# Optimization experiments

Hardware: AMD Instinct MI355X
Metric: run time of the kernel (lower is better)

## Reference

```python
import jax, jax.numpy as jnp
import numpy as np

B, C, N = 2, 256, 4096
H, HD = 8, 32  # num_heads, head_dim; H*HD == C
SCALE = HD ** (-0.5)


def setup_inputs() -> dict:
    key = jax.random.key(0)
    ks = jax.random.split(key, 5)
    return {
        "x": jax.random.normal(ks[0], (B, C, N), dtype=jnp.float32),
        "qkv_w": jax.random.normal(ks[1], (3 * C, C), dtype=jnp.float32) * (C ** -0.5),
        "qkv_b": jax.random.normal(ks[2], (3 * C,), dtype=jnp.float32) * 0.02,
        "out_w": jax.random.normal(ks[3], (C, C), dtype=jnp.float32) * (C ** -0.5),
        "out_b": jax.random.normal(ks[4], (C,), dtype=jnp.float32) * 0.02,
    }


def reference(x, qkv_w, qkv_b, out_w, out_b):
    b, c, n = x.shape
    # 1x1 conv == channel GEMM: [b, 3c, n]
    qkv = jnp.einsum("oc,bcn->bon", qkv_w, x) + qkv_b[None, :, None]
    qkv = qkv.reshape(b, 3, H, c // H, n)
    qkv = jnp.transpose(qkv, (1, 0, 2, 4, 3))  # (3, b, h, n, hd)
    q, k, v = qkv[0], qkv[1], qkv[2]
    attn = jnp.einsum("bhqd,bhkd->bhqk", q, k) * SCALE  # full NxN scores
    attn = jax.nn.softmax(attn, axis=-1)
    out = jnp.einsum("bhqk,bhkd->bhqd", attn, v)
    out = jnp.transpose(out, (0, 1, 3, 2)).reshape(b, c, n)
    out = jnp.einsum("oc,bcn->bon", out_w, out) + out_b[None, :, None]
    return out
```

## Files before the change

kernel.cpp:

```cpp
#include <hip/hip_runtime.h>
#include <math.h>

#define NSEQ 4096
#define QSCL (0.17677669529663687f * 1.4426950408889634f)

typedef __attribute__((ext_vector_type(2))) _Float16 half2v;
typedef __attribute__((ext_vector_type(8))) _Float16 half8;
typedef __attribute__((ext_vector_type(4))) float f32x4;
typedef __attribute__((ext_vector_type(16))) float f32x16;
typedef __attribute__((ext_vector_type(2))) float f32x2;
typedef __attribute__((ext_vector_type(2))) unsigned int u32x2;
typedef __attribute__((ext_vector_type(4))) unsigned int u32x4;

#if __has_builtin(__builtin_amdgcn_exp2f)
#define EXP2(x) __builtin_amdgcn_exp2f(x)
#else
#define EXP2(x) exp2f(x)
#endif

__device__ __forceinline__ half2v pk2(float a, float b) {
  return __builtin_bit_cast(half2v, __builtin_amdgcn_cvt_pkrtz(a, b));
}
__device__ __forceinline__ unsigned pk2u(float a, float b) {
  return __builtin_bit_cast(unsigned, __builtin_amdgcn_cvt_pkrtz(a, b));
}

__device__ __forceinline__ void swap32(unsigned a, unsigned b, unsigned& r0,
                                       unsigned& r1, int lane) {
#if __has_builtin(__builtin_amdgcn_permlane32_swap)
  typedef __attribute__((ext_vector_type(2))) unsigned uint2v;
  uint2v s = __builtin_amdgcn_permlane32_swap(a, b, false, false);
  r0 = s[0];
  r1 = s[1];
#else
  unsigned ax = __shfl_xor((int)a, 32), bx = __shfl_xor((int)b, 32);
  const bool lo = lane < 32;
  r0 = lo ? a : bx;
  r1 = lo ? ax : b;
#endif
}

__global__ __launch_bounds__(256) void prep_all(
    const float* __restrict__ x, const float* __restrict__ qkv_w,
    const float* __restrict__ out_w, _Float16* __restrict__ Xh,
    _Float16* __restrict__ Wqh, _Float16* __restrict__ Wql,
    _Float16* __restrict__ Woh, _Float16* __restrict__ Wol) {
  __shared__ float T[64][68];
  if (blockIdx.z == 2) {
    const int wid = blockIdx.y * 64 + blockIdx.x;
    const int idx = (wid * 256 + threadIdx.x) * 4;
    const int NQ = 768 * 256;
    float4 v;
    _Float16 *dh, *dl;
    int off;
    if (idx < NQ) {
      off = idx;
      v = *(const float4*)(qkv_w + off);
      dh = Wqh;
      dl = Wql;
    } else {
      off = idx - NQ;
      v = *(const float4*)(out_w + off);
      dh = Woh;
      dl = Wol;
    }
    half2v h0 = pk2(v.x, v.y), h1 = pk2(v.z, v.w);
    half2v l0 = pk2(v.x - (float)h0[0], v.y - (float)h0[1]);
    half2v l1 = pk2(v.z - (float)h1[0], v.w - (float)h1[1]);
    u32x2 H, L;
    H[0] = __builtin_bit_cast(unsigned, h0);
    H[1] = __builtin_bit_cast(unsigned, h1);
    L[0] = __builtin_bit_cast(unsigned, l0);
    L[1] = __builtin_bit_cast(unsigned, l1);
    *(u32x2*)(dh + off) = H;
    *(u32x2*)(dl + off) = L;
    return;
  }
  const int b = blockIdx.z, c0 = blockIdx.y * 64, n0 = blockIdx.x * 64;
  const int t = threadIdx.x;
  {
    const int cc = t >> 4, nn = (t & 15) * 4;
    #pragma unroll
    for (int i = 0; i < 4; ++i) {
      float4 v = *(const float4*)(x + ((size_t)(b * 256 + c0 + cc + i * 16)) * NSEQ + n0 + nn);
      *(float4*)&T[cc + i * 16][nn] = v;
    }
  }
  __syncthreads();
  const int nn = t >> 2, cq = t & 3;
  float v[16];
  #pragma unroll
  for (int jj = 0; jj < 16; ++jj) v[jj] = T[cq * 16 + jj][nn];
  half8 hi0, hi1;
  #pragma unroll
  for (int i = 0; i < 4; ++i) {
    half2v h = pk2(v[2 * i], v[2 * i + 1]);
    hi0[2 * i] = h[0]; hi0[2 * i + 1] = h[1];
    half2v h2 = pk2(v[8 + 2 * i], v[8 + 2 * i + 1]);
    hi1[2 * i] = h2[0]; hi1[2 * i + 1] = h2[1];
  }
  const size_t base = ((size_t)b * NSEQ + n0 + nn) * 256 + c0 + cq * 16;
  *(half8*)(Xh + base) = hi0;
  *(half8*)(Xh + base + 8) = hi1;
}

__global__ __launch_bounds__(256) void gemm_qkv(
    const _Float16* __restrict__ Wh, const _Float16* __restrict__ Wl,
    const _Float16* __restrict__ Xh, const float* __restrict__ bias,
    _Float16* __restrict__ Qp, _Float16* __restrict__ Kp,
    _Float16* __restrict__ Vp) {
  const int b = blockIdx.z, n0 = blockIdx.x * 64, m0 = blockIdx.y * 128;
  const int tid = threadIdx.x, w = tid >> 6, lane = tid & 63;
  const int lq = lane & 15, g = lane >> 4;
  const int mw = m0 + w * 32;
  f32x4 acc[2][4] = {};
  const size_t a0 = (size_t)(mw + lq) * 256 + 8 * g;
  const size_t a1 = (size_t)(mw + 16 + lq) * 256 + 8 * g;
  const size_t xrow = ((size_t)b * NSEQ + n0 + lq) * 256 + 8 * g;
  #pragma unroll
  for (int k0 = 0; k0 < 256; k0 += 32) {
    half8 ah0 = *(const half8*)(Wh + a0 + k0);
    half8 ah1 = *(const half8*)(Wh + a1 + k0);
    half8 al0 = *(const half8*)(Wl + a0 + k0);
    half8 al1 = *(const half8*)(Wl + a1 + k0);
    #pragma unroll
    for (int ns = 0; ns < 4; ++ns) {
      half8 bh_ = *(const half8*)(Xh + xrow + (size_t)ns * 16 * 256 + k0);
      acc[0][ns] = __builtin_amdgcn_mfma_f32_16x16x32_f16(ah0, bh_, acc[0][ns], 0, 0, 0);
      acc[0][ns] = __builtin_amdgcn_mfma_f32_16x16x32_f16(al0, bh_, acc[0][ns], 0, 0, 0);
      acc[1][ns] = __builtin_amdgcn_mfma_f32_16x16x32_f16(ah1, bh_, acc[1][ns], 0, 0, 0);
      acc[1][ns] = __builtin_amdgcn_mfma_f32_16x16x32_f16(al1, bh_, acc[1][ns], 0, 0, 0);
    }
  }
  const int seg = mw >> 8;
  const int hh = (mw >> 5) & 7;
  const int bhi = b * 8 + hh;
  #pragma unroll
  for (int ms = 0; ms < 2; ++ms) {
    const int dbase = ms * 16 + 4 * g;
    float4 bi = *(const float4*)(bias + mw + dbase);
    #pragma unroll
    for (int ns = 0; ns < 4; ++ns) {
      const int n = n0 + ns * 16 + lq;
      float v0 = acc[ms][ns][0] + bi.x;
      float v1 = acc[ms][ns][1] + bi.y;
      float v2 = acc[ms][ns][2] + bi.z;
      float v3 = acc[ms][ns][3] + bi.w;
      if (seg == 0) {
        v0 *= QSCL; v1 *= QSCL; v2 *= QSCL; v3 *= QSCL;
        u32x2 H;
        H[0] = pk2u(v0, v1);
        H[1] = pk2u(v2, v3);
        *(u32x2*)(Qp + ((size_t)bhi * NSEQ + n) * 32 + dbase) = H;
      } else if (seg == 1) {
        u32x2 H;
        H[0] = pk2u(v0, v1);
        H[1] = pk2u(v2, v3);
        *(u32x2*)(Kp + ((size_t)bhi * NSEQ + n) * 32 + dbase) = H;
      } else {
        Vp[((size_t)bhi * 32 + dbase + 0) * NSEQ + n] = (_Float16)v0;
        Vp[((size_t)bhi * 32 + dbase + 1) * NSEQ + n] = (_Float16)v1;
        Vp[((size_t)bhi * 32 + dbase + 2) * NSEQ + n] = (_Float16)v2;
        Vp[((size_t)bhi * 32 + dbase + 3) * NSEQ + n] = (_Float16)v3;
      }
    }
  }
}

__global__ __launch_bounds__(256, 2) void attn_part(
    const _Float16* __restrict__ Qp, const _Float16* __restrict__ Kp,
    const _Float16* __restrict__ Vp, _Float16* __restrict__ pp,
    float* __restrict__ lsum) {
  const int b = blockIdx.z, h = blockIdx.y, bh = b * 8 + h;
  const int qt = blockIdx.x & 15, ks_ = blockIdx.x >> 4;
  const int tid = threadIdx.x, w = tid >> 6, lane = tid & 63;
  const int l31 = lane & 31, hw = lane >> 5;
  const int hi8 = hw * 8;
  const int n0 = qt * 256 + w * 64;

  half8 qf[2][2];
  #pragma unroll
  for (int s = 0; s < 2; ++s)
    #pragma unroll
    for (int dh = 0; dh < 2; ++dh)
      qf[s][dh] = *(const half8*)(Qp + ((size_t)bh * NSEQ + n0 + s * 32 + l31) * 32 +
                                  dh * 16 + hi8);

  f32x16 acc[2] = {};
  float lp[2][4] = {};
  const _Float16* Kb = Kp + ((size_t)bh * NSEQ + ks_ * 2048) * 32;
  const _Float16* Vb = Vp + (size_t)bh * 32 * NSEQ + ks_ * 2048;

  half8 kA[4], kB[4];

  auto kload = [&](half8* dst, int t) {
    const int key0 = t * 64;
    #pragma unroll
    for (int kt = 0; kt < 2; ++kt)
      #pragma unroll
      for (int dh = 0; dh < 2; ++dh)
        dst[kt * 2 + dh] = *(const half8*)(Kb + (size_t)(key0 + kt * 32 + l31) * 32 +
                                           dh * 16 + hi8);
  };

  auto compute = [&](const half8* kf, int t) {
    const int key0 = t * 64;
    half8 vf[4];
    #pragma unroll
    for (int c = 0; c < 4; ++c)
      vf[c] = *(const half8*)(Vb + (size_t)l31 * NSEQ + key0 + c * 16 + hi8);
    __builtin_amdgcn_s_setprio(1);
    #pragma unroll
    for (int s = 0; s < 2; ++s) {
      #pragma unroll
      for (int kt = 0; kt < 2; ++kt) {
        f32x16 sc = {0.f, 0.f, 0.f, 0.f, 0.f, 0.f, 0.f, 0.f,
                     0.f, 0.f, 0.f, 0.f, 0.f, 0.f, 0.f, 0.f};
        sc = __builtin_amdgcn_mfma_f32_32x32x16_f16(kf[kt * 2 + 0], qf[s][0], sc, 0, 0, 0);
        sc = __builtin_amdgcn_mfma_f32_32x32x16_f16(kf[kt * 2 + 1], qf[s][1], sc, 0, 0, 0);
        float p[16];
        #pragma unroll
        for (int i = 0; i < 16; ++i) {
          p[i] = EXP2(sc[i]);
          lp[s][i & 3] += p[i];
        }
        #pragma unroll
        for (int cc = 0; cc < 2; ++cc) {
          unsigned A01 = pk2u(p[cc * 8 + 0], p[cc * 8 + 1]);
          unsigned A23 = pk2u(p[cc * 8 + 2], p[cc * 8 + 3]);
          unsigned A45 = pk2u(p[cc * 8 + 4], p[cc * 8 + 5]);
          unsigned A67 = pk2u(p[cc * 8 + 6], p[cc * 8 + 7]);
          unsigned r0, r1, r2, r3;
          swap32(A01, A45, r0, r1, lane);
          swap32(A23, A67, r2, r3, lane);
          u32x4 W;
          W[0] = r0;
          W[1] = r2;
          W[2] = r1;
          W[3] = r3;
          half8 pb = __builtin_bit_cast(half8, W);
          acc[s] = __builtin_amdgcn_mfma_f32_32x32x16_f16(vf[kt * 2 + cc], pb, acc[s], 0, 0, 0);
        }
      }
    }
    __builtin_amdgcn_s_setprio(0);
  };

  kload(kA, 0);
  #pragma unroll 1
  for (int t = 0; t < 32; t += 2) {
    kload(kB, t + 1);
    compute(kA, t);
    kload(kA, t + 2 < 32 ? t + 2 : 31);
    compute(kB, t + 1);
  }

  #pragma unroll
  for (int s = 0; s < 2; ++s) {
    float l = (lp[s][0] + lp[s][1]) + (lp[s][2] + lp[s][3]);
    l += __shfl_xor(l, 32);
    const float inv = 1.f / l;
    const int q = n0 + s * 32 + l31;
    const size_t pbase = ((size_t)(bh * 2 + ks_) * NSEQ + q) * 32;
    #pragma unroll
    for (int rg = 0; rg < 4; ++rg) {
      const int d0 = rg * 8 + 4 * hw;
      float v0 = acc[s][rg * 4 + 0] * inv, v1 = acc[s][rg * 4 + 1] * inv;
      float v2 = acc[s][rg * 4 + 2] * inv, v3 = acc[s][rg * 4 + 3] * inv;
      u32x2 H;
      H[0] = pk2u(v0, v1);
      H[1] = pk2u(v2, v3);
      *(u32x2*)(pp + pbase + d0) = H;
    }
    if (lane < 32) lsum[((size_t)bh * NSEQ + q) * 2 + ks_] = l;
  }
}

__global__ __launch_bounds__(256) void gemm_proj(
    const _Float16* __restrict__ Wh, const _Float16* __restrict__ Wl,
    const _Float16* __restrict__ pp, const float* __restrict__ lsum,
    const float* __restrict__ bias, float* __restrict__ out) {
  const int b = blockIdx.z, n0 = blockIdx.x * 64, m0 = blockIdx.y * 64;
  const int tid = threadIdx.x, w = tid >> 6, lane = tid & 63;
  const int lq = lane & 15, g = lane >> 4;
  const int mw = m0 + w * 16;
  f32x4 acc[4] = {};
  const size_t a0 = (size_t)(mw + lq) * 256 + 8 * g;
  #pragma unroll
  for (int k0 = 0; k0 < 256; k0 += 32) {
    half8 ah = *(const half8*)(Wh + a0 + k0);
    half8 al = *(const half8*)(Wl + a0 + k0);
    const int c = k0 + 8 * g;
    const int hch = c >> 5, d0 = c & 31;
    const int bh = b * 8 + hch;
    #pragma unroll
    for (int ns = 0; ns < 4; ++ns) {
      const int n = n0 + ns * 16 + lq;
      const size_t pb = ((size_t)(bh * 2) * NSEQ + n) * 32 + d0;
      half8 pa = *(const half8*)(pp + pb);
      half8 pbp = *(const half8*)(pp + pb + (size_t)NSEQ * 32);
      f32x2 lv = *(const f32x2*)(lsum + ((size_t)bh * NSEQ + n) * 2);
      const float iv = 1.f / (lv[0] + lv[1]);
      const float w0 = lv[0] * iv, w1 = lv[1] * iv;
      half8 bh_;
      #pragma unroll
      for (int i = 0; i < 4; ++i) {
        float e0 = w0 * (float)pa[2 * i] + w1 * (float)pbp[2 * i];
        float e1 = w0 * (float)pa[2 * i + 1] + w1 * (float)pbp[2 * i + 1];
        half2v hp = pk2(e0, e1);
        bh_[2 * i] = hp[0];
        bh_[2 * i + 1] = hp[1];
      }
      acc[ns] = __builtin_amdgcn_mfma_f32_16x16x32_f16(ah, bh_, acc[ns], 0, 0, 0);
      acc[ns] = __builtin_amdgcn_mfma_f32_16x16x32_f16(al, bh_, acc[ns], 0, 0, 0);
    }
  }
  float4 bi = *(const float4*)(bias + mw + 4 * g);
  #pragma unroll
  for (int ns = 0; ns < 4; ++ns) {
    const int n = n0 + ns * 16 + lq;
    out[((size_t)b * 256 + mw + 4 * g + 0) * NSEQ + n] = acc[ns][0] + bi.x;
    out[((size_t)b * 256 + mw + 4 * g + 1) * NSEQ + n] = acc[ns][1] + bi.y;
    out[((size_t)b * 256 + mw + 4 * g + 2) * NSEQ + n] = acc[ns][2] + bi.z;
    out[((size_t)b * 256 + mw + 4 * g + 3) * NSEQ + n] = acc[ns][3] + bi.w;
  }
}

extern "C" void kernel_launch(void* const* d_in, const int* in_sizes, int n_in,
                              void* d_out, int out_size, void* d_ws, size_t ws_size,
                              hipStream_t stream) {
  const float* x = (const float*)d_in[0];
  const float* qkv_w = (const float*)d_in[1];
  const float* qkv_b = (const float*)d_in[2];
  const float* out_w = (const float*)d_in[3];
  const float* out_b = (const float*)d_in[4];
  float* out = (float*)d_out;

  char* ws = (char*)d_ws;
  _Float16* Vp = (_Float16*)(ws);
  _Float16* Qp = (_Float16*)(ws + (4u << 20));
  _Float16* Kp = (_Float16*)(ws + (8u << 20));
  _Float16* Xh = (_Float16*)(ws + (12u << 20));
  _Float16* pp = (_Float16*)(ws + (16u << 20));
  _Float16* Wqh = (_Float16*)(ws + (28u << 20));
  _Float16* Wql = (_Float16*)(ws + (28u << 20) + (384u << 10));
  _Float16* Woh = (_Float16*)(ws + (28u << 20) + (768u << 10));
  _Float16* Wol = (_Float16*)(ws + (28u << 20) + (896u << 10));
  float* lsum = (float*)(ws + (29u << 20));

  prep_all<<<dim3(NSEQ / 64, 4, 3), 256, 0, stream>>>(x, qkv_w, out_w, Xh,
                                                      Wqh, Wql, Woh, Wol);
  gemm_qkv<<<dim3(NSEQ / 64, 6, 2), 256, 0, stream>>>(Wqh, Wql, Xh, qkv_b,
                                                      Qp, Kp, Vp);
  attn_part<<<dim3(32, 8, 2), 256, 0, stream>>>(Qp, Kp, Vp, pp, lsum);
  gemm_proj<<<dim3(NSEQ / 64, 4, 2), 256, 0, stream>>>(Woh, Wol, pp, lsum,
                                                       out_b, out);
}
```

Before: 101.6 us.

## Fuse input and weight fp16 conversion into the GEMM kernels, drop prep kernel

Removes the separate prep kernel. gemm_qkv now loads fp32 x tiles, converts and transposes them through shared memory, and splits fp32 weights into hi/lo halves in registers on the fly. gemm_proj also converts its fp32 weights inline. This saves one launch and the round trip of the converted tensors through global memory. In exchange, every block redoes the weight conversion and adds shared-memory staging with per-chunk barriers, and the scalar 2-byte shared-memory stores may cause bank conflicts.

```diff
diff --git a/kernel.cpp b/kernel.cpp
--- a/kernel.cpp
+++ b/kernel.cpp
@@ -23,6 +23,20 @@
 }
 __device__ __forceinline__ unsigned pk2u(float a, float b) {
   return __builtin_bit_cast(unsigned, __builtin_amdgcn_cvt_pkrtz(a, b));
+}
+
+__device__ __forceinline__ void cvt_hilo(float4 a, float4 b, half8& hi,
+                                         half8& lo) {
+  half2v h0 = pk2(a.x, a.y), h1 = pk2(a.z, a.w);
+  half2v h2 = pk2(b.x, b.y), h3 = pk2(b.z, b.w);
+  hi[0] = h0[0]; hi[1] = h0[1]; hi[2] = h1[0]; hi[3] = h1[1];
+  hi[4] = h2[0]; hi[5] = h2[1]; hi[6] = h3[0]; hi[7] = h3[1];
+  half2v e0 = pk2(a.x - (float)h0[0], a.y - (float)h0[1]);
+  half2v e1 = pk2(a.z - (float)h1[0], a.w - (float)h1[1]);
+  half2v e2 = pk2(b.x - (float)h2[0], b.y - (float)h2[1]);
+  half2v e3 = pk2(b.z - (float)h3[0], b.w - (float)h3[1]);
+  lo[0] = e0[0]; lo[1] = e0[1]; lo[2] = e1[0]; lo[3] = e1[1];
+  lo[4] = e2[0]; lo[5] = e2[1]; lo[6] = e3[0]; lo[7] = e3[1];
 }
 
 __device__ __forceinline__ void swap32(unsigned a, unsigned b, unsigned& r0,
@@ -40,96 +54,52 @@
 #endif
 }
 
-__global__ __launch_bounds__(256) void prep_all(
-    const float* __restrict__ x, const float* __restrict__ qkv_w,
-    const float* __restrict__ out_w, _Float16* __restrict__ Xh,
-    _Float16* __restrict__ Wqh, _Float16* __restrict__ Wql,
-    _Float16* __restrict__ Woh, _Float16* __restrict__ Wol) {
-  __shared__ float T[64][68];
-  if (blockIdx.z == 2) {
-    const int wid = blockIdx.y * 64 + blockIdx.x;
-    const int idx = (wid * 256 + threadIdx.x) * 4;
-    const int NQ = 768 * 256;
-    float4 v;
-    _Float16 *dh, *dl;
-    int off;
-    if (idx < NQ) {
-      off = idx;
-      v = *(const float4*)(qkv_w + off);
-      dh = Wqh;
-      dl = Wql;
-    } else {
-      off = idx - NQ;
-      v = *(const float4*)(out_w + off);
-      dh = Woh;
-      dl = Wol;
-    }
-    half2v h0 = pk2(v.x, v.y), h1 = pk2(v.z, v.w);
-    half2v l0 = pk2(v.x - (float)h0[0], v.y - (float)h0[1]);
-    half2v l1 = pk2(v.z - (float)h1[0], v.w - (float)h1[1]);
-    u32x2 H, L;
-    H[0] = __builtin_bit_cast(unsigned, h0);
-    H[1] = __builtin_bit_cast(unsigned, h1);
-    L[0] = __builtin_bit_cast(unsigned, l0);
-    L[1] = __builtin_bit_cast(unsigned, l1);
-    *(u32x2*)(dh + off) = H;
-    *(u32x2*)(dl + off) = L;
-    return;
-  }
-  const int b = blockIdx.z, c0 = blockIdx.y * 64, n0 = blockIdx.x * 64;
-  const int t = threadIdx.x;
-  {
-    const int cc = t >> 4, nn = (t & 15) * 4;
-    #pragma unroll
-    for (int i = 0; i < 4; ++i) {
-      float4 v = *(const float4*)(x + ((size_t)(b * 256 + c0 + cc + i * 16)) * NSEQ + n0 + nn);
-      *(float4*)&T[cc + i * 16][nn] = v;
-    }
-  }
-  __syncthreads();
-  const int nn = t >> 2, cq = t & 3;
-  float v[16];
-  #pragma unroll
-  for (int jj = 0; jj < 16; ++jj) v[jj] = T[cq * 16 + jj][nn];
-  half8 hi0, hi1;
-  #pragma unroll
-  for (int i = 0; i < 4; ++i) {
-    half2v h = pk2(v[2 * i], v[2 * i + 1]);
-    hi0[2 * i] = h[0]; hi0[2 * i + 1] = h[1];
-    half2v h2 = pk2(v[8 + 2 * i], v[8 + 2 * i + 1]);
-    hi1[2 * i] = h2[0]; hi1[2 * i + 1] = h2[1];
-  }
-  const size_t base = ((size_t)b * NSEQ + n0 + nn) * 256 + c0 + cq * 16;
-  *(half8*)(Xh + base) = hi0;
-  *(half8*)(Xh + base + 8) = hi1;
-}
-
 __global__ __launch_bounds__(256) void gemm_qkv(
-    const _Float16* __restrict__ Wh, const _Float16* __restrict__ Wl,
-    const _Float16* __restrict__ Xh, const float* __restrict__ bias,
-    _Float16* __restrict__ Qp, _Float16* __restrict__ Kp,
-    _Float16* __restrict__ Vp) {
+    const float* __restrict__ Wf, const float* __restrict__ x,
+    const float* __restrict__ bias, _Float16* __restrict__ Qp,
+    _Float16* __restrict__ Kp, _Float16* __restrict__ Vp) {
+  __shared__ _Float16 XT[64][72];
   const int b = blockIdx.z, n0 = blockIdx.x * 64, m0 = blockIdx.y * 128;
   const int tid = threadIdx.x, w = tid >> 6, lane = tid & 63;
   const int lq = lane & 15, g = lane >> 4;
   const int mw = m0 + w * 32;
+  const int cc = tid >> 4, nn = (tid & 15) * 4;
   f32x4 acc[2][4] = {};
-  const size_t a0 = (size_t)(mw + lq) * 256 + 8 * g;
-  const size_t a1 = (size_t)(mw + 16 + lq) * 256 + 8 * g;
-  const size_t xrow = ((size_t)b * NSEQ + n0 + lq) * 256 + 8 * g;
-  #pragma unroll
-  for (int k0 = 0; k0 < 256; k0 += 32) {
-    half8 ah0 = *(const half8*)(Wh + a0 + k0);
-    half8 ah1 = *(const half8*)(Wh + a1 + k0);
-    half8 al0 = *(const half8*)(Wl + a0 + k0);
-    half8 al1 = *(const half8*)(Wl + a1 + k0);
-    #pragma unroll
-    for (int ns = 0; ns < 4; ++ns) {
-      half8 bh_ = *(const half8*)(Xh + xrow + (size_t)ns * 16 * 256 + k0);
-      acc[0][ns] = __builtin_amdgcn_mfma_f32_16x16x32_f16(ah0, bh_, acc[0][ns], 0, 0, 0);
-      acc[0][ns] = __builtin_amdgcn_mfma_f32_16x16x32_f16(al0, bh_, acc[0][ns], 0, 0, 0);
-      acc[1][ns] = __builtin_amdgcn_mfma_f32_16x16x32_f16(ah1, bh_, acc[1][ns], 0, 0, 0);
-      acc[1][ns] = __builtin_amdgcn_mfma_f32_16x16x32_f16(al1, bh_, acc[1][ns], 0, 0, 0);
+  const size_t wr0 = (size_t)(mw + lq) * 256 + 8 * g;
+  const size_t wr1 = (size_t)(mw + 16 + lq) * 256 + 8 * g;
+
+  for (int kc = 0; kc < 4; ++kc) {
+    if (kc) __syncthreads();
+    #pragma unroll
+    for (int i = 0; i < 4; ++i) {
+      const int c = cc + 16 * i;
+      float4 v = *(const float4*)(
+          x + ((size_t)(b * 256 + kc * 64 + c)) * NSEQ + n0 + nn);
+      XT[nn + 0][c] = (_Float16)v.x;
+      XT[nn + 1][c] = (_Float16)v.y;
+      XT[nn + 2][c] = (_Float16)v.z;
+      XT[nn + 3][c] = (_Float16)v.w;
+    }
+    __syncthreads();
+    #pragma unroll
+    for (int kh = 0; kh < 2; ++kh) {
+      const int k0 = kc * 64 + kh * 32;
+      float4 wa0 = *(const float4*)(Wf + wr0 + k0);
+      float4 wa1 = *(const float4*)(Wf + wr0 + k0 + 4);
+      float4 wb0 = *(const float4*)(Wf + wr1 + k0);
+      float4 wb1 = *(const float4*)(Wf + wr1 + k0 + 4);
+      half8 ah0, al0, ah1, al1;
+      cvt_hilo(wa0, wa1, ah0, al0);
+      cvt_hilo(wb0, wb1, ah1, al1);
+      const int dk = kh * 32 + 8 * g;
+      #pragma unroll
+      for (int ns = 0; ns < 4; ++ns) {
+        half8 bh_ = *(const half8*)&XT[ns * 16 + lq][dk];
+        acc[0][ns] = __builtin_amdgcn_mfma_f32_16x16x32_f16(ah0, bh_, acc[0][ns], 0, 0, 0);
+        acc[0][ns] = __builtin_amdgcn_mfma_f32_16x16x32_f16(al0, bh_, acc[0][ns], 0, 0, 0);
+        acc[1][ns] = __builtin_amdgcn_mfma_f32_16x16x32_f16(ah1, bh_, acc[1][ns], 0, 0, 0);
+        acc[1][ns] = __builtin_amdgcn_mfma_f32_16x16x32_f16(al1, bh_, acc[1][ns], 0, 0, 0);
+      }
     }
   }
   const int seg = mw >> 8;
@@ -277,19 +247,21 @@
 }
 
 __global__ __launch_bounds__(256) void gemm_proj(
-    const _Float16* __restrict__ Wh, const _Float16* __restrict__ Wl,
-    const _Float16* __restrict__ pp, const float* __restrict__ lsum,
-    const float* __restrict__ bias, float* __restrict__ out) {
+    const float* __restrict__ Wf, const _Float16* __restrict__ pp,
+    const float* __restrict__ lsum, const float* __restrict__ bias,
+    float* __restrict__ out) {
   const int b = blockIdx.z, n0 = blockIdx.x * 64, m0 = blockIdx.y * 64;
   const int tid = threadIdx.x, w = tid >> 6, lane = tid & 63;
   const int lq = lane & 15, g = lane >> 4;
   const int mw = m0 + w * 16;
   f32x4 acc[4] = {};
-  const size_t a0 = (size_t)(mw + lq) * 256 + 8 * g;
+  const size_t wr = (size_t)(mw + lq) * 256 + 8 * g;
   #pragma unroll
   for (int k0 = 0; k0 < 256; k0 += 32) {
-    half8 ah = *(const half8*)(Wh + a0 + k0);
-    half8 al = *(const half8*)(Wl + a0 + k0);
+    float4 wa0 = *(const float4*)(Wf + wr + k0);
+    float4 wa1 = *(const float4*)(Wf + wr + k0 + 4);
+    half8 ah, al;
+    cvt_hilo(wa0, wa1, ah, al);
     const int c = k0 + 8 * g;
     const int hch = c >> 5, d0 = c & 31;
     const int bh = b * 8 + hch;
@@ -340,19 +312,12 @@
   _Float16* Vp = (_Float16*)(ws);
   _Float16* Qp = (_Float16*)(ws + (4u << 20));
   _Float16* Kp = (_Float16*)(ws + (8u << 20));
-  _Float16* Xh = (_Float16*)(ws + (12u << 20));
-  _Float16* pp = (_Float16*)(ws + (16u << 20));
-  _Float16* Wqh = (_Float16*)(ws + (28u << 20));
-  _Float16* Wql = (_Float16*)(ws + (28u << 20) + (384u << 10));
-  _Float16* Woh = (_Float16*)(ws + (28u << 20) + (768u << 10));
-  _Float16* Wol = (_Float16*)(ws + (28u << 20) + (896u << 10));
-  float* lsum = (float*)(ws + (29u << 20));
-
-  prep_all<<<dim3(NSEQ / 64, 4, 3), 256, 0, stream>>>(x, qkv_w, out_w, Xh,
-                                                      Wqh, Wql, Woh, Wol);
-  gemm_qkv<<<dim3(NSEQ / 64, 6, 2), 256, 0, stream>>>(Wqh, Wql, Xh, qkv_b,
+  _Float16* pp = (_Float16*)(ws + (12u << 20));
+  float* lsum = (float*)(ws + (20u << 20));
+
+  gemm_qkv<<<dim3(NSEQ / 64, 6, 2), 256, 0, stream>>>(qkv_w, x, qkv_b,
                                                       Qp, Kp, Vp);
   attn_part<<<dim3(32, 8, 2), 256, 0, stream>>>(Qp, Kp, Vp, pp, lsum);
-  gemm_proj<<<dim3(NSEQ / 64, 4, 2), 256, 0, stream>>>(Woh, Wol, pp, lsum,
+  gemm_proj<<<dim3(NSEQ / 64, 4, 2), 256, 0, stream>>>(out_w, pp, lsum,
                                                        out_b, out);
 }
```

New measurement: 92.37 us. 1.1x faster.
